# Kernel optimization log

Hardware: AMD Instinct MI355X
Metric: run time of the kernel (lower is better)

Reference implementation:

```python
import jax, jax.numpy as jnp
import numpy as np

B = 4096
N_OBJS = 128        # num_objs
D_OBJ = 64
D_MODEL = 256
OTHER_START = 64    # other_start_dim
D_OBS = OTHER_START + N_OBJS * D_OBJ  # 8256
HIDDEN = 256
ACT_DIM = 2
NEG_INF = -1e9


def setup_inputs() -> dict:
    key = jax.random.key(0)
    ks = jax.random.split(key, 16)
    obs = jax.random.normal(ks[0], (B, D_OBS), dtype=jnp.float32)
    mask = jax.random.randint(ks[1], (B, N_OBJS), 0, 2).astype(jnp.float32)
    inputs = jnp.concatenate([obs, mask], axis=1)  # [B, D_OBS + N_OBJS]

    def orth(k, n, gain):
        a = jax.random.normal(k, (n, n))
        q, _ = jnp.linalg.qr(a)
        return (gain * q).astype(jnp.float32)

    g = np.sqrt(2.0)
    params = {
        "W_emb": jax.random.normal(ks[2], (D_OBJ, D_MODEL), dtype=jnp.float32) * 0.05,
        "b_emb": jnp.zeros((D_MODEL,), dtype=jnp.float32),
        "Uq": orth(ks[3], D_MODEL, g),
        "Ur": orth(ks[4], D_MODEL, g),
        "Ua": jax.random.normal(ks[5], (D_MODEL, 1), dtype=jnp.float32) * 0.1,
        "W1p": jax.random.normal(ks[6], (OTHER_START + D_MODEL, HIDDEN), dtype=jnp.float32) * 0.05,
        "b1p": jnp.zeros((HIDDEN,), dtype=jnp.float32),
        "W2p": jax.random.normal(ks[7], (HIDDEN, HIDDEN), dtype=jnp.float32) * 0.05,
        "b2p": jnp.zeros((HIDDEN,), dtype=jnp.float32),
        "W3p": jax.random.normal(ks[8], (HIDDEN, 2 * ACT_DIM), dtype=jnp.float32) * 0.05,
        "b3p": jnp.zeros((2 * ACT_DIM,), dtype=jnp.float32),
        "W1v": jax.random.normal(ks[9], (OTHER_START + D_MODEL, HIDDEN), dtype=jnp.float32) * 0.05,
        "b1v": jnp.zeros((HIDDEN,), dtype=jnp.float32),
        "W2v": jax.random.normal(ks[10], (HIDDEN, HIDDEN), dtype=jnp.float32) * 0.05,
        "b2v": jnp.zeros((HIDDEN,), dtype=jnp.float32),
        "W3v": jax.random.normal(ks[11], (HIDDEN, 1), dtype=jnp.float32) * 0.05,
        "b3v": jnp.zeros((1,), dtype=jnp.float32),
    }
    return {"inputs": inputs, **params}


def reference(inputs, W_emb, b_emb, Uq, Ur, Ua,
              W1p, b1p, W2p, b2p, W3p, b3p,
              W1v, b1v, W2v, b2v, W3v, b3v):
    obs = inputs[:, :D_OBS]
    mask = inputs[:, D_OBS:]                              # [B, N]
    others = obs[:, OTHER_START:].reshape(-1, N_OBJS, D_OBJ)
    # Conv1D kernel_size=1 == per-object linear
    x_others = others @ W_emb + b_emb                     # [B, N, d]
    x_real = x_others * mask[:, :, None]
    query = x_real.sum(axis=1) / (mask.sum(axis=1, keepdims=True) + 1e-5)  # [B, d]
    m = jnp.tanh((query @ Uq)[:, None, :] + x_real @ Ur)  # [B, N, d]
    logits = jnp.squeeze(m @ Ua, axis=-1) + (1.0 - mask) * NEG_INF
    attn = jax.nn.softmax(logits, axis=-1)                # [B, N]
    pooled = jnp.einsum("bn,bnd->bd", attn, x_others)     # [B, d]
    state = jnp.concatenate([obs[:, :OTHER_START], pooled], axis=1)

    xp = jnp.tanh(state @ W1p + b1p)
    xp = jnp.tanh(xp @ W2p + b2p)
    xp = xp @ W3p + b3p                                   # [B, 2*act_dim]
    mean = xp[:, :ACT_DIM]
    action = jnp.tanh(mean)

    xv = jnp.tanh(state @ W1v + b1v)
    xv = jnp.tanh(xv @ W2v + b2v)
    value = xv @ W3v + b3v                                # [B, 1]

    return jnp.concatenate([value, action, attn], axis=1)  # [B, 1+act_dim+N]
```

## Files before the change

### kernel.cpp

```cpp
#include <hip/hip_runtime.h>

typedef __attribute__((ext_vector_type(8))) short short8;
typedef __attribute__((ext_vector_type(4))) short short4v;
typedef __attribute__((ext_vector_type(4))) float f32x4;

#define B_ROWS 4096
#define IN_STRIDE 8384
#define OUT_STRIDE 131

static __device__ __forceinline__ short f2bf(float f) {
  unsigned u = __float_as_uint(f);
  u = u + 0x7FFFu + ((u >> 16) & 1u);
  return (short)(u >> 16);
}
static __device__ __forceinline__ float bf2f(short s) {
  return __uint_as_float(((unsigned)(unsigned short)s) << 16);
}
static __device__ __forceinline__ float fast_tanh(float x) {
  float e = __builtin_amdgcn_exp2f(x * 2.8853900817779268f);
  return 1.0f - 2.0f * __builtin_amdgcn_rcpf(e + 1.0f);
}

__global__ __launch_bounds__(256) void prep_kernel(
    const float* __restrict__ W_emb, const float* __restrict__ b_emb,
    const float* __restrict__ Uq, const float* __restrict__ Ur,
    const float* __restrict__ W1p, const float* __restrict__ W1v,
    const float* __restrict__ W2p, const float* __restrict__ W2v,
    const float* __restrict__ b1p, const float* __restrict__ b1v,
    const float* __restrict__ b2p, const float* __restrict__ b2v,
    short* __restrict__ WembUq, short* __restrict__ WembUrT,
    short* __restrict__ Wemb16, float* __restrict__ bUq, float* __restrict__ bUr,
    float* __restrict__ b1cat, float* __restrict__ b2cat,
    short* __restrict__ W1T, short* __restrict__ W2T)
{
  const int blk = blockIdx.x, t = threadIdx.x;
  if (blk < 128) {
    const int d = blk & 63;
    const float* U = (blk < 64) ? Uq : Ur;
    float acc = 0.f;
    for (int k = 0; k < 256; ++k) acc += W_emb[d * 256 + k] * U[k * 256 + t];
    if (blk < 64) WembUq[d * 256 + t] = f2bf(acc);
    else          WembUrT[t * 64 + d] = f2bf(acc);
  } else if (blk == 128) {
    float aq = 0.f, ar = 0.f;
    for (int k = 0; k < 256; ++k) {
      float b = b_emb[k];
      aq += b * Uq[k * 256 + t];
      ar += b * Ur[k * 256 + t];
    }
    bUq[t] = aq; bUr[t] = ar;
  } else if (blk == 129) {
    b1cat[t] = b1p[t]; b1cat[256 + t] = b1v[t];
    b2cat[t] = b2p[t]; b2cat[256 + t] = b2v[t];
    for (int i = 0; i < 64; ++i) Wemb16[i * 256 + t] = f2bf(W_emb[i * 256 + t]);
  } else if (blk < 770) {
    const int e = (blk - 130) * 256 + t;
    const int n = e / 320, k = e - n * 320;
    const float v = (n < 256) ? W1p[k * 256 + n] : W1v[k * 256 + (n - 256)];
    W1T[e] = f2bf(v);
  } else {
    const int e = (blk - 770) * 256 + t;
    const int n = e >> 8, k = e & 255;
    const float v = (n < 256) ? W2p[k * 256 + n] : W2v[k * 256 + (n - 256)];
    W2T[e] = f2bf(v);
  }
}

__global__ __launch_bounds__(256) void attn_kernel(
    const float* __restrict__ in, const short* __restrict__ BT,
    const short* __restrict__ WembUq, const short* __restrict__ Wemb16,
    const float* __restrict__ bUq, const float* __restrict__ bUr,
    const float* __restrict__ Ua, const float* __restrict__ b_emb,
    float* __restrict__ out, short* __restrict__ state)
{
  __shared__ short Blds[256 * 64];
  __shared__ float ua_lds[256];
  __shared__ float mask_lds[128];
  __shared__ float osum_p[4][64];
  __shared__ float osum_tot[64];
  __shared__ float qU_lds[256];
  __shared__ float logit_lds[128];
  __shared__ float obar_p[4][64];
  __shared__ float obar_tot[64];

  const int t = threadIdx.x, w = t >> 6, l = t & 63;
  const int q = l >> 4, r16 = l & 15;
  const int row = blockIdx.x;
  const float* __restrict__ xrow = in + (size_t)row * IN_STRIDE;
  const float* __restrict__ others = xrow + 64;
  const float* __restrict__ maskp = xrow + 8256;

  float m0 = maskp[l], m1 = maskp[64 + l];
  float4 pv[2][4];
#pragma unroll
  for (int ml = 0; ml < 2; ++ml) {
    const int gr = (2 * w + ml) * 16 + r16;
    const float4* p = (const float4*)(others + gr * 64 + q * 8);
    pv[ml][0] = p[0]; pv[ml][1] = p[1]; pv[ml][2] = p[8]; pv[ml][3] = p[9];
  }
  {
    const int4* src = (const int4*)BT;
#pragma unroll
    for (int it = 0; it < 8; ++it) {
      int cl = it * 256 + t;
      int n = cl >> 3, c = cl & 7;
      int4 v = src[cl];
      *(int4*)&Blds[n * 64 + ((c ^ (n & 7)) << 3)] = v;
    }
    ua_lds[t] = Ua[t];
    if (w == 0) { mask_lds[l] = m0; mask_lds[64 + l] = m1; }
  }

  float S = m0 + m1;
#pragma unroll
  for (int d = 1; d < 64; d <<= 1) S += __shfl_xor(S, d);

  short8 afrag[2][2];
  float osA[8], osB[8];
#pragma unroll
  for (int j = 0; j < 8; ++j) { osA[j] = 0.f; osB[j] = 0.f; }
#pragma unroll
  for (int ml = 0; ml < 2; ++ml) {
    const int midx = 32 * w + 16 * ml + r16;
    const float mk = (w < 2) ? __shfl(m0, midx) : __shfl(m1, midx & 63);
    float fa[8] = {pv[ml][0].x, pv[ml][0].y, pv[ml][0].z, pv[ml][0].w,
                   pv[ml][1].x, pv[ml][1].y, pv[ml][1].z, pv[ml][1].w};
    float fb[8] = {pv[ml][2].x, pv[ml][2].y, pv[ml][2].z, pv[ml][2].w,
                   pv[ml][3].x, pv[ml][3].y, pv[ml][3].z, pv[ml][3].w};
    short8 s0, s1;
#pragma unroll
    for (int j = 0; j < 8; ++j) {
      float va = fa[j] * mk, vb = fb[j] * mk;
      osA[j] += va; osB[j] += vb;
      s0[j] = f2bf(va); s1[j] = f2bf(vb);
    }
    afrag[ml][0] = s0; afrag[ml][1] = s1;
  }
#pragma unroll
  for (int d = 1; d < 16; d <<= 1) {
#pragma unroll
    for (int j = 0; j < 8; ++j) {
      osA[j] += __shfl_xor(osA[j], d);
      osB[j] += __shfl_xor(osB[j], d);
    }
  }
  if (r16 == 0) {
#pragma unroll
    for (int j = 0; j < 8; ++j) {
      osum_p[w][q * 8 + j] = osA[j];
      osum_p[w][q * 8 + 32 + j] = osB[j];
    }
  }
  __syncthreads();

  if (t < 64) osum_tot[t] = osum_p[0][t] + osum_p[1][t] + osum_p[2][t] + osum_p[3][t];
  __syncthreads();

  {
    float acc = 0.f;
    for (int d = 0; d < 64; ++d)
      acc += osum_tot[d] * bf2f(WembUq[d * 256 + t]);
    const float rS = __builtin_amdgcn_rcpf(S + 1e-5f);
    qU_lds[t] = (acc + S * bUq[t]) * rS + bUr[t];
  }
  __syncthreads();

  const f32x4 fzero = {0.f, 0.f, 0.f, 0.f};
  f32x4 lp[2];
  lp[0] = fzero; lp[1] = fzero;
  for (int nt = 0; nt < 16; ++nt) {
    const int col = nt * 16 + r16;
    const float qv = qU_lds[col];
    const float uav = ua_lds[col];
    const int sw = col & 7;
    const short8 bf0 = *(const short8*)&Blds[col * 64 + (((q) ^ sw) << 3)];
    const short8 bf1 = *(const short8*)&Blds[col * 64 + (((q + 4) ^ sw) << 3)];
#pragma unroll
    for (int ml = 0; ml < 2; ++ml) {
      f32x4 acc = fzero;
      acc = __builtin_amdgcn_mfma_f32_16x16x32_bf16(afrag[ml][0], bf0, acc, 0, 0, 0);
      acc = __builtin_amdgcn_mfma_f32_16x16x32_bf16(afrag[ml][1], bf1, acc, 0, 0, 0);
#pragma unroll
      for (int rr = 0; rr < 4; ++rr) {
        lp[ml][rr] += uav * fast_tanh(qv + acc[rr]);
      }
    }
  }
#pragma unroll
  for (int ml = 0; ml < 2; ++ml) {
#pragma unroll
    for (int rr = 0; rr < 4; ++rr) {
      float v = lp[ml][rr];
      v += __shfl_xor(v, 1); v += __shfl_xor(v, 2);
      v += __shfl_xor(v, 4); v += __shfl_xor(v, 8);
      lp[ml][rr] = v;
    }
  }
  if (r16 == 0) {
#pragma unroll
    for (int ml = 0; ml < 2; ++ml) {
#pragma unroll
      for (int rr = 0; rr < 4; ++rr) {
        const int n = (2 * w + ml) * 16 + q * 4 + rr;
        float lg = lp[ml][rr];
        if (mask_lds[n] == 0.f) lg = -1e9f;
        logit_lds[n] = lg;
      }
    }
  }
  __syncthreads();

  float a0, a1;
  {
    float l0 = logit_lds[l], l1 = logit_lds[64 + l];
    float mx = fmaxf(l0, l1);
#pragma unroll
    for (int d = 1; d < 64; d <<= 1) mx = fmaxf(mx, __shfl_xor(mx, d));
    float e0 = __builtin_amdgcn_exp2f((l0 - mx) * 1.4426950408889634f);
    float e1 = __builtin_amdgcn_exp2f((l1 - mx) * 1.4426950408889634f);
    float s = e0 + e1;
#pragma unroll
    for (int d = 1; d < 64; d <<= 1) s += __shfl_xor(s, d);
    float rs = __builtin_amdgcn_rcpf(s);
    a0 = e0 * rs; a1 = e1 * rs;
    float* __restrict__ orow = out + (size_t)row * OUT_STRIDE;
    if (w == 0) orow[3 + l] = a0;
    if (w == 1) orow[3 + 64 + l] = a1;
  }

  {
    float ob[16];
#pragma unroll
    for (int j = 0; j < 16; ++j) ob[j] = 0.f;
#pragma unroll
    for (int ml = 0; ml < 2; ++ml) {
      const int idx = 32 * w + 16 * ml + r16;
      const float av = (w < 2) ? __shfl(a0, idx) : __shfl(a1, idx & 63);
      const short8 f0 = afrag[ml][0], f1 = afrag[ml][1];
#pragma unroll
      for (int j = 0; j < 8; ++j) {
        ob[j] += av * bf2f(f0[j]);
        ob[8 + j] += av * bf2f(f1[j]);
      }
    }
#pragma unroll
    for (int d = 1; d < 16; d <<= 1) {
#pragma unroll
      for (int j = 0; j < 16; ++j) ob[j] += __shfl_xor(ob[j], d);
    }
    if (r16 == 0) {
#pragma unroll
      for (int j = 0; j < 8; ++j) {
        obar_p[w][q * 8 + j] = ob[j];
        obar_p[w][q * 8 + 32 + j] = ob[8 + j];
      }
    }
  }
  __syncthreads();
  if (t < 64) obar_tot[t] = obar_p[0][t] + obar_p[1][t] + obar_p[2][t] + obar_p[3][t];
  __syncthreads();

  {
    float acc = 0.f;
    for (int d = 0; d < 64; ++d)
      acc += obar_tot[d] * bf2f(Wemb16[d * 256 + t]);
    short* __restrict__ srow = state + (size_t)row * 320;
    srow[64 + t] = f2bf(acc + b_emb[t]);
    if (t < 64) srow[t] = f2bf(xrow[t]);
  }
}

__global__ __launch_bounds__(256) void mlp_gemm(
    const short* __restrict__ A, int lda, const short* __restrict__ BT,
    const float* __restrict__ bias, short* __restrict__ C, int ldc,
    int K, int split)
{
  __shared__ short Alds[64 * 32];
  __shared__ short Blds[128 * 32];
  const int t = threadIdx.x, l = t & 63, wid = t >> 6;
  const int bm = blockIdx.x, bn = blockIdx.y;
  const int acol0 = (split && bn >= ((int)gridDim.y >> 1)) ? K : 0;
  const int wm = wid >> 1, wn = wid & 1;
  const int q = l >> 4, r16 = l & 15;
  const f32x4 fzero = {0.f, 0.f, 0.f, 0.f};
  f32x4 acc[2][4];
#pragma unroll
  for (int fm = 0; fm < 2; ++fm)
#pragma unroll
    for (int fn = 0; fn < 4; ++fn) acc[fm][fn] = fzero;

  for (int kt = 0; kt < K; kt += 32) {
    {
      const int rrow = t >> 2, c = t & 3;
      int4 va = *(const int4*)&A[(size_t)(bm * 64 + rrow) * lda + acol0 + kt + c * 8];
      *(int4*)&Alds[rrow * 32 + ((c ^ (rrow & 3)) << 3)] = va;
#pragma unroll
      for (int e = 0; e < 2; ++e) {
        const int ei = t + e * 256;
        const int br = ei >> 2, bc = ei & 3;
        int4 vb = *(const int4*)&BT[(size_t)(bn * 128 + br) * K + kt + bc * 8];
        *(int4*)&Blds[br * 32 + ((bc ^ (br & 3)) << 3)] = vb;
      }
    }
    __syncthreads();
    short8 af[2], bf[4];
#pragma unroll
    for (int fm = 0; fm < 2; ++fm) {
      const int ar = wm * 32 + fm * 16 + r16;
      af[fm] = *(const short8*)&Alds[ar * 32 + ((q ^ (ar & 3)) << 3)];
    }
#pragma unroll
    for (int fn = 0; fn < 4; ++fn) {
      const int br = wn * 64 + fn * 16 + r16;
      bf[fn] = *(const short8*)&Blds[br * 32 + ((q ^ (br & 3)) << 3)];
    }
#pragma unroll
    for (int fm = 0; fm < 2; ++fm)
#pragma unroll
      for (int fn = 0; fn < 4; ++fn)
        acc[fm][fn] = __builtin_amdgcn_mfma_f32_16x16x32_bf16(af[fm], bf[fn], acc[fm][fn], 0, 0, 0);
    __syncthreads();
  }

#pragma unroll
  for (int fn = 0; fn < 4; ++fn) {
    const int col = bn * 128 + wn * 64 + fn * 16 + r16;
    const float bv = bias[col];
#pragma unroll
    for (int fm = 0; fm < 2; ++fm) {
#pragma unroll
      for (int rr = 0; rr < 4; ++rr) {
        const int crow = bm * 64 + wm * 32 + fm * 16 + q * 4 + rr;
        C[(size_t)crow * ldc + col] = f2bf(fast_tanh(acc[fm][fn][rr] + bv));
      }
    }
  }
}

__global__ __launch_bounds__(256) void head_kernel(
    const short* __restrict__ H2, const float* __restrict__ W3p,
    const float* __restrict__ b3p, const float* __restrict__ W3v,
    const float* __restrict__ b3v, float* __restrict__ out)
{
  const int t = threadIdx.x, w = t >> 6, l = t & 63;
  const int row = blockIdx.x * 4 + w;
  const short* __restrict__ h = H2 + (size_t)row * 512;
  float vp0 = 0.f, vp1 = 0.f, vv = 0.f;
#pragma unroll
  for (int i = 0; i < 4; ++i) {
    const int k = i * 64 + l;
    const float hp = bf2f(h[k]);
    const float hv = bf2f(h[256 + k]);
    vp0 += hp * W3p[k * 4 + 0];
    vp1 += hp * W3p[k * 4 + 1];
    vv += hv * W3v[k];
  }
#pragma unroll
  for (int d = 1; d < 64; d <<= 1) {
    vp0 += __shfl_xor(vp0, d);
    vp1 += __shfl_xor(vp1, d);
    vv += __shfl_xor(vv, d);
  }
  if (l == 0) {
    float* __restrict__ orow = out + (size_t)row * OUT_STRIDE;
    orow[0] = vv + b3v[0];
    orow[1] = fast_tanh(vp0 + b3p[0]);
    orow[2] = fast_tanh(vp1 + b3p[1]);
  }
}

extern "C" void kernel_launch(void* const* d_in, const int* in_sizes, int n_in,
                              void* d_out, int out_size, void* d_ws, size_t ws_size,
                              hipStream_t stream) {
  (void)in_sizes; (void)n_in; (void)out_size; (void)ws_size;
  const float* inp   = (const float*)d_in[0];
  const float* W_emb = (const float*)d_in[1];
  const float* b_emb = (const float*)d_in[2];
  const float* Uq    = (const float*)d_in[3];
  const float* Ur    = (const float*)d_in[4];
  const float* Ua    = (const float*)d_in[5];
  const float* W1p   = (const float*)d_in[6];
  const float* b1p   = (const float*)d_in[7];
  const float* W2p   = (const float*)d_in[8];
  const float* b2p   = (const float*)d_in[9];
  const float* W3p   = (const float*)d_in[10];
  const float* b3p   = (const float*)d_in[11];
  const float* W1v   = (const float*)d_in[12];
  const float* b1v   = (const float*)d_in[13];
  const float* W2v   = (const float*)d_in[14];
  const float* b2v   = (const float*)d_in[15];
  const float* W3v   = (const float*)d_in[16];
  const float* b3v   = (const float*)d_in[17];

  char* ws = (char*)d_ws;
  short* WembUq  = (short*)(ws + 0);
  short* WembUrT = (short*)(ws + 32768);
  short* Wemb16  = (short*)(ws + 65536);
  float* bUq     = (float*)(ws + 98304);
  float* bUr     = (float*)(ws + 99328);
  float* b1cat   = (float*)(ws + 100352);
  float* b2cat   = (float*)(ws + 102400);
  short* W1T     = (short*)(ws + 104448);
  short* W2T     = (short*)(ws + 432128);
  short* state   = (short*)(ws + 694272);
  short* H1      = (short*)(ws + 3315712);
  short* H2      = (short*)(ws + 7510016);

  prep_kernel<<<dim3(1282), dim3(256), 0, stream>>>(
      W_emb, b_emb, Uq, Ur, W1p, W1v, W2p, W2v, b1p, b1v, b2p, b2v,
      WembUq, WembUrT, Wemb16, bUq, bUr, b1cat, b2cat, W1T, W2T);

  attn_kernel<<<dim3(4096), dim3(256), 0, stream>>>(
      inp, WembUrT, WembUq, Wemb16, bUq, bUr, Ua, b_emb, (float*)d_out, state);

  mlp_gemm<<<dim3(64, 4), dim3(256), 0, stream>>>(state, 320, W1T, b1cat, H1, 512, 320, 0);
  mlp_gemm<<<dim3(64, 4), dim3(256), 0, stream>>>(H1, 512, W2T, b2cat, H2, 512, 256, 1);

  head_kernel<<<dim3(1024), dim3(256), 0, stream>>>(H2, W3p, b3p, W3v, b3v, (float*)d_out);
}
```

Measured before the change: 111.2 us.

## Process four batch rows per attention block to share staged Ur weights

The attention kernel now runs 1024-thread blocks, each handling four batch rows, so the 32KB bf16 Ur weight tile staged into LDS is loaded once per four rows instead of once per row. All per-row scratch arrays gain a row dimension. The query bias is folded into the MFMA accumulator's initial value, and the small 64-term dot loops are unrolled. In exchange, larger blocks with block-wide barriers couple four rows' progress, and the launch bound of 1024 threads with min 8 blocks may constrain register allocation.

```diff
diff --git a/kernel.cpp b/kernel.cpp
--- a/kernel.cpp
+++ b/kernel.cpp
@@ -66,7 +66,7 @@
   }
 }
 
-__global__ __launch_bounds__(256) void attn_kernel(
+__global__ __launch_bounds__(1024, 8) void attn_kernel(
     const float* __restrict__ in, const short* __restrict__ BT,
     const short* __restrict__ WembUq, const short* __restrict__ Wemb16,
     const float* __restrict__ bUq, const float* __restrict__ bUr,
@@ -75,17 +75,20 @@
 {
   __shared__ short Blds[256 * 64];
   __shared__ float ua_lds[256];
-  __shared__ float mask_lds[128];
-  __shared__ float osum_p[4][64];
-  __shared__ float osum_tot[64];
-  __shared__ float qU_lds[256];
-  __shared__ float logit_lds[128];
-  __shared__ float obar_p[4][64];
-  __shared__ float obar_tot[64];
-
-  const int t = threadIdx.x, w = t >> 6, l = t & 63;
+  __shared__ float mask_lds[4][128];
+  __shared__ float osum_p[4][4][64];
+  __shared__ float osum_tot[4][64];
+  __shared__ float qU_lds[4][256];
+  __shared__ float logit_lds[4][128];
+  __shared__ float obar_p[4][4][64];
+  __shared__ float obar_tot[4][64];
+
+  const int t = threadIdx.x, l = t & 63;
+  const int rw = t >> 8;
+  const int w4 = (t >> 6) & 3;
+  const int tl = t & 255;
   const int q = l >> 4, r16 = l & 15;
-  const int row = blockIdx.x;
+  const int row = blockIdx.x * 4 + rw;
   const float* __restrict__ xrow = in + (size_t)row * IN_STRIDE;
   const float* __restrict__ others = xrow + 64;
   const float* __restrict__ maskp = xrow + 8256;
@@ -94,21 +97,21 @@
   float4 pv[2][4];
 #pragma unroll
   for (int ml = 0; ml < 2; ++ml) {
-    const int gr = (2 * w + ml) * 16 + r16;
+    const int gr = (2 * w4 + ml) * 16 + r16;
     const float4* p = (const float4*)(others + gr * 64 + q * 8);
     pv[ml][0] = p[0]; pv[ml][1] = p[1]; pv[ml][2] = p[8]; pv[ml][3] = p[9];
   }
   {
     const int4* src = (const int4*)BT;
 #pragma unroll
-    for (int it = 0; it < 8; ++it) {
-      int cl = it * 256 + t;
+    for (int it = 0; it < 2; ++it) {
+      int cl = it * 1024 + t;
       int n = cl >> 3, c = cl & 7;
       int4 v = src[cl];
       *(int4*)&Blds[n * 64 + ((c ^ (n & 7)) << 3)] = v;
     }
-    ua_lds[t] = Ua[t];
-    if (w == 0) { mask_lds[l] = m0; mask_lds[64 + l] = m1; }
+    if (t < 256) ua_lds[t] = Ua[t];
+    if (w4 == 0) { mask_lds[rw][l] = m0; mask_lds[rw][64 + l] = m1; }
   }
 
   float S = m0 + m1;
@@ -121,8 +124,8 @@
   for (int j = 0; j < 8; ++j) { osA[j] = 0.f; osB[j] = 0.f; }
 #pragma unroll
   for (int ml = 0; ml < 2; ++ml) {
-    const int midx = 32 * w + 16 * ml + r16;
-    const float mk = (w < 2) ? __shfl(m0, midx) : __shfl(m1, midx & 63);
+    const int midx = 32 * w4 + 16 * ml + r16;
+    const float mk = (w4 < 2) ? __shfl(m0, midx) : __shfl(m1, midx & 63);
     float fa[8] = {pv[ml][0].x, pv[ml][0].y, pv[ml][0].z, pv[ml][0].w,
                    pv[ml][1].x, pv[ml][1].y, pv[ml][1].z, pv[ml][1].w};
     float fb[8] = {pv[ml][2].x, pv[ml][2].y, pv[ml][2].z, pv[ml][2].w,
@@ -147,21 +150,23 @@
   if (r16 == 0) {
 #pragma unroll
     for (int j = 0; j < 8; ++j) {
-      osum_p[w][q * 8 + j] = osA[j];
-      osum_p[w][q * 8 + 32 + j] = osB[j];
-    }
-  }
-  __syncthreads();
-
-  if (t < 64) osum_tot[t] = osum_p[0][t] + osum_p[1][t] + osum_p[2][t] + osum_p[3][t];
+      osum_p[rw][w4][q * 8 + j] = osA[j];
+      osum_p[rw][w4][q * 8 + 32 + j] = osB[j];
+    }
+  }
+  __syncthreads();
+
+  if (tl < 64)
+    osum_tot[rw][tl] = osum_p[rw][0][tl] + osum_p[rw][1][tl] + osum_p[rw][2][tl] + osum_p[rw][3][tl];
   __syncthreads();
 
   {
     float acc = 0.f;
+#pragma unroll 16
     for (int d = 0; d < 64; ++d)
-      acc += osum_tot[d] * bf2f(WembUq[d * 256 + t]);
+      acc += osum_tot[rw][d] * bf2f(WembUq[d * 256 + tl]);
     const float rS = __builtin_amdgcn_rcpf(S + 1e-5f);
-    qU_lds[t] = (acc + S * bUq[t]) * rS + bUr[t];
+    qU_lds[rw][tl] = (acc + S * bUq[tl]) * rS + bUr[tl];
   }
   __syncthreads();
 
@@ -170,19 +175,19 @@
   lp[0] = fzero; lp[1] = fzero;
   for (int nt = 0; nt < 16; ++nt) {
     const int col = nt * 16 + r16;
-    const float qv = qU_lds[col];
+    const float qv = qU_lds[rw][col];
     const float uav = ua_lds[col];
     const int sw = col & 7;
     const short8 bf0 = *(const short8*)&Blds[col * 64 + (((q) ^ sw) << 3)];
     const short8 bf1 = *(const short8*)&Blds[col * 64 + (((q + 4) ^ sw) << 3)];
 #pragma unroll
     for (int ml = 0; ml < 2; ++ml) {
-      f32x4 acc = fzero;
+      f32x4 acc = {qv, qv, qv, qv};
       acc = __builtin_amdgcn_mfma_f32_16x16x32_bf16(afrag[ml][0], bf0, acc, 0, 0, 0);
       acc = __builtin_amdgcn_mfma_f32_16x16x32_bf16(afrag[ml][1], bf1, acc, 0, 0, 0);
 #pragma unroll
       for (int rr = 0; rr < 4; ++rr) {
-        lp[ml][rr] += uav * fast_tanh(qv + acc[rr]);
+        lp[ml][rr] += uav * fast_tanh(acc[rr]);
       }
     }
   }
@@ -201,10 +206,10 @@
     for (int ml = 0; ml < 2; ++ml) {
 #pragma unroll
       for (int rr = 0; rr < 4; ++rr) {
-        const int n = (2 * w + ml) * 16 + q * 4 + rr;
+        const int n = (2 * w4 + ml) * 16 + q * 4 + rr;
         float lg = lp[ml][rr];
-        if (mask_lds[n] == 0.f) lg = -1e9f;
-        logit_lds[n] = lg;
+        if (mask_lds[rw][n] == 0.f) lg = -1e9f;
+        logit_lds[rw][n] = lg;
       }
     }
   }
@@ -212,7 +217,7 @@
 
   float a0, a1;
   {
-    float l0 = logit_lds[l], l1 = logit_lds[64 + l];
+    float l0 = logit_lds[rw][l], l1 = logit_lds[rw][64 + l];
     float mx = fmaxf(l0, l1);
 #pragma unroll
     for (int d = 1; d < 64; d <<= 1) mx = fmaxf(mx, __shfl_xor(mx, d));
@@ -224,8 +229,8 @@
     float rs = __builtin_amdgcn_rcpf(s);
     a0 = e0 * rs; a1 = e1 * rs;
     float* __restrict__ orow = out + (size_t)row * OUT_STRIDE;
-    if (w == 0) orow[3 + l] = a0;
-    if (w == 1) orow[3 + 64 + l] = a1;
+    if (w4 == 0) orow[3 + l] = a0;
+    if (w4 == 1) orow[3 + 64 + l] = a1;
   }
 
   {
@@ -234,8 +239,8 @@
     for (int j = 0; j < 16; ++j) ob[j] = 0.f;
 #pragma unroll
     for (int ml = 0; ml < 2; ++ml) {
-      const int idx = 32 * w + 16 * ml + r16;
-      const float av = (w < 2) ? __shfl(a0, idx) : __shfl(a1, idx & 63);
+      const int idx = 32 * w4 + 16 * ml + r16;
+      const float av = (w4 < 2) ? __shfl(a0, idx) : __shfl(a1, idx & 63);
       const short8 f0 = afrag[ml][0], f1 = afrag[ml][1];
 #pragma unroll
       for (int j = 0; j < 8; ++j) {
@@ -251,22 +256,24 @@
     if (r16 == 0) {
 #pragma unroll
       for (int j = 0; j < 8; ++j) {
-        obar_p[w][q * 8 + j] = ob[j];
-        obar_p[w][q * 8 + 32 + j] = ob[8 + j];
-      }
-    }
-  }
-  __syncthreads();
-  if (t < 64) obar_tot[t] = obar_p[0][t] + obar_p[1][t] + obar_p[2][t] + obar_p[3][t];
+        obar_p[rw][w4][q * 8 + j] = ob[j];
+        obar_p[rw][w4][q * 8 + 32 + j] = ob[8 + j];
+      }
+    }
+  }
+  __syncthreads();
+  if (tl < 64)
+    obar_tot[rw][tl] = obar_p[rw][0][tl] + obar_p[rw][1][tl] + obar_p[rw][2][tl] + obar_p[rw][3][tl];
   __syncthreads();
 
   {
     float acc = 0.f;
+#pragma unroll 16
     for (int d = 0; d < 64; ++d)
-      acc += obar_tot[d] * bf2f(Wemb16[d * 256 + t]);
+      acc += obar_tot[rw][d] * bf2f(Wemb16[d * 256 + tl]);
     short* __restrict__ srow = state + (size_t)row * 320;
-    srow[64 + t] = f2bf(acc + b_emb[t]);
-    if (t < 64) srow[t] = f2bf(xrow[t]);
+    srow[64 + tl] = f2bf(acc + b_emb[tl]);
+    if (tl < 64) srow[tl] = f2bf(xrow[tl]);
   }
 }
 
@@ -410,7 +417,7 @@
       W_emb, b_emb, Uq, Ur, W1p, W1v, W2p, W2v, b1p, b1v, b2p, b2v,
       WembUq, WembUrT, Wemb16, bUq, bUr, b1cat, b2cat, W1T, W2T);
 
-  attn_kernel<<<dim3(4096), dim3(256), 0, stream>>>(
+  attn_kernel<<<dim3(1024), dim3(1024), 0, stream>>>(
       inp, WembUrT, WembUq, Wemb16, bUq, bUr, Ua, b_emb, (float*)d_out, state);
 
   mlp_gemm<<<dim3(64, 4), dim3(256), 0, stream>>>(state, 320, W1T, b1cat, H1, 512, 320, 0);
```

Measured after the change: 368.4 us. 3.31x slower.

## Halve attention kernel LDS by staging Ur weights in two halves

Applied to the files above, without the earlier changes.

The attention kernel now keeps only half of the 256x64 bf16 Ur^T matrix in LDS at a time, loading the second half after the first 8 column tiles with extra barriers. The reduction scratch buffers are shared between the two reductions. Together these cut shared memory per block from over 32KB to about 16KB so more blocks can be resident per CU. The query bias is folded into the MFMA accumulator init, and the small dot loops are unrolled. The cost is a mid-kernel reload with two more barriers, which partly serializes the weight fetch.

```diff
diff --git a/kernel.cpp b/kernel.cpp
--- a/kernel.cpp
+++ b/kernel.cpp
@@ -73,15 +73,13 @@
     const float* __restrict__ Ua, const float* __restrict__ b_emb,
     float* __restrict__ out, short* __restrict__ state)
 {
-  __shared__ short Blds[256 * 64];
+  __shared__ short Bhalf[128 * 64];
   __shared__ float ua_lds[256];
   __shared__ float mask_lds[128];
-  __shared__ float osum_p[4][64];
-  __shared__ float osum_tot[64];
+  __shared__ float red_p[4][64];
+  __shared__ float red_tot[64];
   __shared__ float qU_lds[256];
   __shared__ float logit_lds[128];
-  __shared__ float obar_p[4][64];
-  __shared__ float obar_tot[64];
 
   const int t = threadIdx.x, w = t >> 6, l = t & 63;
   const int q = l >> 4, r16 = l & 15;
@@ -101,11 +99,11 @@
   {
     const int4* src = (const int4*)BT;
 #pragma unroll
-    for (int it = 0; it < 8; ++it) {
+    for (int it = 0; it < 4; ++it) {
       int cl = it * 256 + t;
       int n = cl >> 3, c = cl & 7;
       int4 v = src[cl];
-      *(int4*)&Blds[n * 64 + ((c ^ (n & 7)) << 3)] = v;
+      *(int4*)&Bhalf[n * 64 + ((c ^ (n & 7)) << 3)] = v;
     }
     ua_lds[t] = Ua[t];
     if (w == 0) { mask_lds[l] = m0; mask_lds[64 + l] = m1; }
@@ -147,19 +145,20 @@
   if (r16 == 0) {
 #pragma unroll
     for (int j = 0; j < 8; ++j) {
-      osum_p[w][q * 8 + j] = osA[j];
-      osum_p[w][q * 8 + 32 + j] = osB[j];
-    }
-  }
-  __syncthreads();
-
-  if (t < 64) osum_tot[t] = osum_p[0][t] + osum_p[1][t] + osum_p[2][t] + osum_p[3][t];
+      red_p[w][q * 8 + j] = osA[j];
+      red_p[w][q * 8 + 32 + j] = osB[j];
+    }
+  }
+  __syncthreads();
+
+  if (t < 64) red_tot[t] = red_p[0][t] + red_p[1][t] + red_p[2][t] + red_p[3][t];
   __syncthreads();
 
   {
     float acc = 0.f;
+#pragma unroll 16
     for (int d = 0; d < 64; ++d)
-      acc += osum_tot[d] * bf2f(WembUq[d * 256 + t]);
+      acc += red_tot[d] * bf2f(WembUq[d * 256 + t]);
     const float rS = __builtin_amdgcn_rcpf(S + 1e-5f);
     qU_lds[t] = (acc + S * bUq[t]) * rS + bUr[t];
   }
@@ -168,21 +167,37 @@
   const f32x4 fzero = {0.f, 0.f, 0.f, 0.f};
   f32x4 lp[2];
   lp[0] = fzero; lp[1] = fzero;
-  for (int nt = 0; nt < 16; ++nt) {
-    const int col = nt * 16 + r16;
-    const float qv = qU_lds[col];
-    const float uav = ua_lds[col];
-    const int sw = col & 7;
-    const short8 bf0 = *(const short8*)&Blds[col * 64 + (((q) ^ sw) << 3)];
-    const short8 bf1 = *(const short8*)&Blds[col * 64 + (((q + 4) ^ sw) << 3)];
-#pragma unroll
-    for (int ml = 0; ml < 2; ++ml) {
-      f32x4 acc = fzero;
-      acc = __builtin_amdgcn_mfma_f32_16x16x32_bf16(afrag[ml][0], bf0, acc, 0, 0, 0);
-      acc = __builtin_amdgcn_mfma_f32_16x16x32_bf16(afrag[ml][1], bf1, acc, 0, 0, 0);
-#pragma unroll
-      for (int rr = 0; rr < 4; ++rr) {
-        lp[ml][rr] += uav * fast_tanh(qv + acc[rr]);
+#pragma unroll
+  for (int h = 0; h < 2; ++h) {
+    if (h == 1) {
+      __syncthreads();
+      const int4* src = (const int4*)BT + 1024;
+#pragma unroll
+      for (int it = 0; it < 4; ++it) {
+        int cl = it * 256 + t;
+        int n = cl >> 3, c = cl & 7;
+        int4 v = src[cl];
+        *(int4*)&Bhalf[n * 64 + ((c ^ (n & 7)) << 3)] = v;
+      }
+      __syncthreads();
+    }
+    for (int nt = 0; nt < 8; ++nt) {
+      const int colL = nt * 16 + r16;
+      const int colG = h * 128 + colL;
+      const float qv = qU_lds[colG];
+      const float uav = ua_lds[colG];
+      const int sw = colL & 7;
+      const short8 bf0 = *(const short8*)&Bhalf[colL * 64 + (((q) ^ sw) << 3)];
+      const short8 bf1 = *(const short8*)&Bhalf[colL * 64 + (((q + 4) ^ sw) << 3)];
+#pragma unroll
+      for (int ml = 0; ml < 2; ++ml) {
+        f32x4 acc = {qv, qv, qv, qv};
+        acc = __builtin_amdgcn_mfma_f32_16x16x32_bf16(afrag[ml][0], bf0, acc, 0, 0, 0);
+        acc = __builtin_amdgcn_mfma_f32_16x16x32_bf16(afrag[ml][1], bf1, acc, 0, 0, 0);
+#pragma unroll
+        for (int rr = 0; rr < 4; ++rr) {
+          lp[ml][rr] += uav * fast_tanh(acc[rr]);
+        }
       }
     }
   }
@@ -248,22 +263,24 @@
 #pragma unroll
       for (int j = 0; j < 16; ++j) ob[j] += __shfl_xor(ob[j], d);
     }
+    __syncthreads();
     if (r16 == 0) {
 #pragma unroll
       for (int j = 0; j < 8; ++j) {
-        obar_p[w][q * 8 + j] = ob[j];
-        obar_p[w][q * 8 + 32 + j] = ob[8 + j];
-      }
-    }
-  }
-  __syncthreads();
-  if (t < 64) obar_tot[t] = obar_p[0][t] + obar_p[1][t] + obar_p[2][t] + obar_p[3][t];
+        red_p[w][q * 8 + j] = ob[j];
+        red_p[w][q * 8 + 32 + j] = ob[8 + j];
+      }
+    }
+  }
+  __syncthreads();
+  if (t < 64) red_tot[t] = red_p[0][t] + red_p[1][t] + red_p[2][t] + red_p[3][t];
   __syncthreads();
 
   {
     float acc = 0.f;
+#pragma unroll 16
     for (int d = 0; d < 64; ++d)
-      acc += obar_tot[d] * bf2f(Wemb16[d * 256 + t]);
+      acc += red_tot[d] * bf2f(Wemb16[d * 256 + t]);
     short* __restrict__ srow = state + (size_t)row * 320;
     srow[64 + t] = f2bf(acc + b_emb[t]);
     if (t < 64) srow[t] = f2bf(xrow[t]);
```

Measured after the change: 139.2 us. +25.2%, slower.
